# Kernel tuning notes

Hardware: AMD Instinct MI355X
Metric: run time of the kernel (lower is better)

## Reference

```python
import jax, jax.numpy as jnp
import numpy as np

NUM_HEADS = 8
EPS = 1e-12  # torch F.normalize default eps


def setup_inputs() -> dict:
    key = jax.random.key(0)
    k0, k1, k2, k3 = jax.random.split(key, 4)
    b, c, d, h, w = 2, 64, 8, 128, 128
    x = jax.random.normal(k0, (b, c, d, h, w), dtype=jnp.float32)
    # 1x1x1 conv weights stored as [out, in]; depthwise 3x3x3 as [out, 1, kd, kh, kw]
    w_qkv = jax.random.normal(k1, (3 * c, c), dtype=jnp.float32) * 0.05
    w_dw = jax.random.normal(k2, (3 * c, 1, 3, 3, 3), dtype=jnp.float32) * 0.05
    temperature = jnp.ones((NUM_HEADS, 1, 1), dtype=jnp.float32)
    w_proj = jax.random.normal(k3, (c, c), dtype=jnp.float32) * 0.05
    return {"x": x, "w_qkv": w_qkv, "w_dw": w_dw, "temperature": temperature, "w_proj": w_proj}


def _l2norm(t):
    # F.normalize(t, dim=-1): t / max(||t||, eps)
    n = jnp.sqrt(jnp.sum(t * t, axis=-1, keepdims=True))
    return t / jnp.maximum(n, EPS)


def reference(x, w_qkv, w_dw, temperature, w_proj):
    b, c, d, h, w = x.shape
    heads = NUM_HEADS
    ch = c // heads  # per-head channel dim
    # 1x1x1 conv (pointwise) -> einsum over channels
    qkv = jnp.einsum('bcdhw,oc->bodhw', x, w_qkv)
    # depthwise 3x3x3 conv, padding 1 (SAME), groups = 3*c
    qkv = jax.lax.conv_general_dilated(
        qkv, w_dw, window_strides=(1, 1, 1), padding=[(1, 1)] * 3,
        feature_group_count=3 * c,
        dimension_numbers=('NCDHW', 'OIDHW', 'NCDHW'))
    q, k, v = jnp.split(qkv, 3, axis=1)
    n = d * h * w
    q = q.reshape(b, heads, ch, n)
    k = k.reshape(b, heads, ch, n)
    v = v.reshape(b, heads, ch, n)
    q = _l2norm(q)
    k = _l2norm(k)
    # channel-channel attention: [b, heads, ch, ch]
    attn = jnp.einsum('bhcn,bhen->bhce', q, k) * temperature
    attn = jax.nn.softmax(attn, axis=-1)
    out = jnp.einsum('bhce,bhen->bhcn', attn, v)
    out = out.reshape(b, c, d, h, w)
    out = jnp.einsum('bcdhw,oc->bodhw', out, w_proj)
    return out
```

## Files before the change

kernel.cpp:

```cpp
#include <hip/hip_runtime.h>
#include <math.h>

#define NPOS 131072
#define GC 128

typedef __attribute__((ext_vector_type(8))) short short8v;
typedef __attribute__((ext_vector_type(4))) float f32x4;

__device__ __forceinline__ void bf16split(float x, unsigned short& hi, unsigned short& lo) {
  unsigned u = __float_as_uint(x);
  hi = (unsigned short)(u >> 16);
  float hif = __uint_as_float(u & 0xffff0000u);
  float l = x - hif;
  lo = (unsigned short)(__float_as_uint(l) >> 16);
}

__global__ void k_prep(const float* __restrict__ w_qkv, unsigned short* __restrict__ whi,
                       unsigned short* __restrict__ wlo) {
  int idx = blockIdx.x * 256 + threadIdx.x;
  if (idx < 12288) {
    int j = idx & 7, l = (idx >> 3) & 63, ks = (idx >> 9) & 1, ot = (idx >> 10) & 3,
        g = idx >> 12;
    int out = ot * 16 + (l & 15);
    int k = ks * 32 + (l >> 4) * 8 + j;
    bf16split(w_qkv[(g * 64 + out) * 64 + k], whi[idx], wlo[idx]);
  }
}

__device__ __forceinline__ void pw_body(const float* __restrict__ gin,
                                        const short8v (*ahi)[2], const short8v (*alo)[2],
                                        float* __restrict__ gout, int tid) {
  __shared__ __align__(16) float xl[64][66];
  const int lane = tid & 63;
  const int wid = tid >> 6;
  const int f4 = tid & 15;
#pragma unroll
  for (int r = 0; r < 4; ++r) {
    int ch2 = (r * 256 + tid) >> 4;
    *(float4*)&xl[ch2][f4 * 4] = *(const float4*)&gin[(size_t)ch2 * NPOS + f4 * 4];
  }
  __syncthreads();
  const int prow = lane & 15, kgrp = lane >> 4;
  const int pos = wid * 16 + prow;
  short8v bh[2], bl[2];
#pragma unroll
  for (int ks = 0; ks < 2; ++ks)
#pragma unroll
    for (int j = 0; j < 8; ++j) {
      unsigned short h, lo16;
      bf16split(xl[ks * 32 + kgrp * 8 + j][pos], h, lo16);
      bh[ks][j] = (short)h;
      bl[ks][j] = (short)lo16;
    }
  f32x4 D[4];
#pragma unroll
  for (int ot = 0; ot < 4; ++ot) {
    f32x4 d = {0.f, 0.f, 0.f, 0.f};
#pragma unroll
    for (int ks = 0; ks < 2; ++ks) {
      d = __builtin_amdgcn_mfma_f32_16x16x32_bf16(ahi[ot][ks], bh[ks], d, 0, 0, 0);
      d = __builtin_amdgcn_mfma_f32_16x16x32_bf16(ahi[ot][ks], bl[ks], d, 0, 0, 0);
      d = __builtin_amdgcn_mfma_f32_16x16x32_bf16(alo[ot][ks], bh[ks], d, 0, 0, 0);
    }
    D[ot] = d;
  }
  __syncthreads();
#pragma unroll
  for (int ot = 0; ot < 4; ++ot)
#pragma unroll
    for (int jj = 0; jj < 4; ++jj)
      xl[ot * 16 + kgrp * 4 + jj][pos] = D[ot][jj];
  __syncthreads();
#pragma unroll
  for (int r = 0; r < 4; ++r) {
    int row = (r * 256 + tid) >> 4;
    *(float4*)&gout[(size_t)row * NPOS + f4 * 4] = *(const float4*)&xl[row][f4 * 4];
  }
}

__global__ __launch_bounds__(256) void k_pw_mfma(const float* __restrict__ x,
                                                 const unsigned short* __restrict__ whi,
                                                 const unsigned short* __restrict__ wlo,
                                                 float* __restrict__ pre) {
  const int id = blockIdx.x;
  const int sid = (id & 7) * 512 + (id >> 3);
  const int b = sid >> 11;
  const int p0 = (sid & 2047) * 64;
  const int lane = threadIdx.x & 63;
  short8v ahi[4][2], alo[4][2];
#pragma unroll
  for (int ot = 0; ot < 4; ++ot)
#pragma unroll
    for (int ks = 0; ks < 2; ++ks) {
      int fi = ((ot * 2 + ks) * 64 + lane) * 8;
      ahi[ot][ks] = *(const short8v*)&whi[fi];
      alo[ot][ks] = *(const short8v*)&wlo[fi];
    }
  pw_body(x + ((size_t)b * 64) * NPOS + p0, ahi, alo,
          pre + ((size_t)b * 64) * NPOS + p0, threadIdx.x);
}

__device__ __forceinline__ void stage_tile(float (*t)[10][40], const float* __restrict__ in,
                                           int h0, int w0, int tid) {
  for (int i = tid; i < 800; i += 256) {
    int j = i & 7, row = i >> 3;
    int h = row % 10, dpl = row / 10;
    int dd = dpl - 1, hh = h0 + h - 1;
    float4 v = make_float4(0.f, 0.f, 0.f, 0.f);
    if (dd >= 0 && dd < 8 && hh >= 0 && hh < 128)
      v = *(const float4*)&in[((size_t)dd * 128 + hh) * 128 + (w0 + j * 4)];
    *(float4*)&t[dpl][h][4 + j * 4] = v;
  }
  for (int i = tid; i < 200; i += 256) {
    int side = i & 1, row = i >> 1;
    int h = row % 10, dpl = row / 10;
    int dd = dpl - 1, hh = h0 + h - 1;
    int ww = side ? (w0 + 32) : (w0 - 1);
    float v = 0.f;
    if (dd >= 0 && dd < 8 && hh >= 0 && hh < 128 && ww >= 0 && ww < 128)
      v = in[((size_t)dd * 128 + hh) * 128 + ww];
    t[dpl][h][side ? 36 : 3] = v;
  }
}

__device__ __forceinline__ void conv_droll(const float (*t)[10][40], const float* wk,
                                           int hl, int wl, float* acc) {
#pragma unroll
  for (int d = 0; d < 8; ++d) acc[d] = 0.f;
#pragma unroll
  for (int dpl = 0; dpl < 10; ++dpl) {
#pragma unroll
    for (int kh = 0; kh < 3; ++kh) {
#pragma unroll
      for (int kw = 0; kw < 3; ++kw) {
        float f = t[dpl][hl + kh][3 + wl + kw];
#pragma unroll
        for (int kd = 0; kd < 3; ++kd) {
          const int d = dpl - kd;
          if (d >= 0 && d < 8)
            acc[d] = fmaf(f, wk[(kd * 3 + kh) * 3 + kw], acc[d]);
        }
      }
    }
  }
}

__global__ __launch_bounds__(256) void k_dw(const float* __restrict__ pre,
                                            const float* __restrict__ w_dw,
                                            float* __restrict__ conv,
                                            float* __restrict__ nsq, int g) {
  const int id = blockIdx.x;
  const int sid = (id & 7) * 1024 + (id >> 3);
  const int z = sid >> 6, r = sid & 63, by = r >> 2, bx = r & 3;
  const int b = z >> 6;
  const int c = z & 63;
  const int h0 = by * 8;
  const int w0 = bx * 32;
  __shared__ float t[10][10][40];
  __shared__ float red[4];
  const int tid = threadIdx.y * 32 + threadIdx.x;
  stage_tile(t, pre + ((size_t)b * 64 + c) * NPOS, h0, w0, tid);
  float wk[27];
#pragma unroll
  for (int i = 0; i < 27; ++i) wk[i] = w_dw[(g * 64 + c) * 27 + i];
  __syncthreads();
  const int wl = threadIdx.x, hl = threadIdx.y;
  float acc[8];
  conv_droll(t, wk, hl, wl, acc);
  float* outp = conv + ((size_t)b * 64 + c) * NPOS + (size_t)(h0 + hl) * 128 + (w0 + wl);
  float nsum = 0.f;
#pragma unroll
  for (int d = 0; d < 8; ++d) {
    outp[(size_t)d * 16384] = acc[d];
    nsum = fmaf(acc[d], acc[d], nsum);
  }
  if (nsq) {
    const int lane = tid & 63, wv = tid >> 6;
    float v = nsum;
    v += __shfl_down(v, 32); v += __shfl_down(v, 16); v += __shfl_down(v, 8);
    v += __shfl_down(v, 4);  v += __shfl_down(v, 2);  v += __shfl_down(v, 1);
    if (lane == 0) red[wv] = v;
    __syncthreads();
    if (tid == 0) {
      const int blk = by * 4 + bx;
      nsq[((size_t)b * 64 + c) * 64 + blk] = red[0] + red[1] + red[2] + red[3];
    }
  }
}

__global__ __launch_bounds__(256) void k_gramS(const float* __restrict__ qconv,
                                               const float* __restrict__ kconv,
                                               float* __restrict__ partialS) {
  const int chunk = blockIdx.x;
  const int bh = blockIdx.y;
  const int b = bh >> 3, head = bh & 7;
  const int tid = threadIdx.x;
  const size_t base = ((size_t)b * 64 + head * 8) * NPOS + (size_t)chunk * 1024 + tid;
  const float* qb = qconv + base;
  const float* kb = kconv + base;
  float S[64];
#pragma unroll
  for (int i = 0; i < 64; ++i) S[i] = 0.f;
#pragma unroll
  for (int it = 0; it < 4; ++it) {
    const size_t off = (size_t)it * 256;
    float qv[8], kv[8];
#pragma unroll
    for (int c = 0; c < 8; ++c) qv[c] = qb[(size_t)c * NPOS + off];
#pragma unroll
    for (int e = 0; e < 8; ++e) kv[e] = kb[(size_t)e * NPOS + off];
#pragma unroll
    for (int c = 0; c < 8; ++c)
#pragma unroll
      for (int e = 0; e < 8; ++e) S[c * 8 + e] = fmaf(qv[c], kv[e], S[c * 8 + e]);
  }
#pragma unroll
  for (int i = 0; i < 64; ++i) asm volatile("" : "+v"(S[i]));

  const int lane = tid & 63, wv = tid >> 6;
#define BSTEP(src, dst, n, s)                                        \
  {                                                                  \
    const bool hi_ = (lane >> (s)) & 1;                              \
    _Pragma("unroll")                                                \
    for (int i_ = 0; i_ < (n); ++i_) {                               \
      float send_ = hi_ ? src[i_] : src[i_ + (n)];                   \
      float mine_ = hi_ ? src[i_ + (n)] : src[i_];                   \
      dst[i_] = mine_ + __shfl_xor(send_, 1 << (s));                 \
    }                                                                \
  }
  float v32[32], v16[16], v8[8], v4[4], v2[2], v1[1];
  BSTEP(S,   v32, 32, 0)
  BSTEP(v32, v16, 16, 1)
  BSTEP(v16, v8,   8, 2)
  BSTEP(v8,  v4,   4, 3)
  BSTEP(v4,  v2,   2, 4)
  BSTEP(v2,  v1,   1, 5)
#undef BSTEP
  const int idx = ((lane & 1) << 5) | ((lane & 2) << 3) | ((lane & 4) << 1) |
                  ((lane & 8) >> 1) | ((lane & 16) >> 3) | ((lane & 32) >> 5);
  __shared__ float red[4][64];
  red[wv][idx] = v1[0];
  __syncthreads();
  if (tid < 64) {
    float s = red[0][tid] + red[1][tid] + red[2][tid] + red[3][tid];
    partialS[((size_t)bh * GC + chunk) * 64 + tid] = s;
  }
}

__global__ void k_attn(const float* __restrict__ partialS, const float* __restrict__ nqp,
                       const float* __restrict__ nkp, const float* __restrict__ temp,
                       float* __restrict__ A) {
  const int bh = blockIdx.x;
  const int b = bh >> 3, head = bh & 7;
  const int tid = threadIdx.x;
  __shared__ float sums[80];
  if (tid < 64) {
    float s = 0.f;
    const float* pp = partialS + (size_t)bh * GC * 64 + tid;
    for (int j = 0; j < GC; ++j) s += pp[j * 64];
    sums[tid] = s;
  } else if (tid < 72) {
    const int e = tid - 64;
    float s = 0.f;
    const float* pp = nkp + ((size_t)b * 64 + head * 8 + e) * 64;
    for (int j = 0; j < 64; ++j) s += pp[j];
    sums[64 + e] = s;
  } else if (tid < 80) {
    const int c = tid - 72;
    float s = 0.f;
    const float* pp = nqp + ((size_t)b * 64 + head * 8 + c) * 64;
    for (int j = 0; j < 64; ++j) s += pp[j];
    sums[72 + c] = s;
  }
  __syncthreads();
  if (tid < 8) {
    const int c = tid;
    float tp = temp[head];
    float qd = fmaxf(sqrtf(sums[72 + c]), 1e-12f);
    float vals[8];
    float mx = -1e30f;
#pragma unroll
    for (int e = 0; e < 8; ++e) {
      float kd = fmaxf(sqrtf(sums[64 + e]), 1e-12f);
      vals[e] = sums[c * 8 + e] / (qd * kd) * tp;
      mx = fmaxf(mx, vals[e]);
    }
    float den = 0.f;
#pragma unroll
    for (int e = 0; e < 8; ++e) { vals[e] = expf(vals[e] - mx); den += vals[e]; }
#pragma unroll
    for (int e = 0; e < 8; ++e) A[bh * 64 + c * 8 + e] = vals[e] / den;
  }
}

__global__ void k_M(const float* __restrict__ w_proj, const float* __restrict__ A,
                    unsigned short* __restrict__ Mhi, unsigned short* __restrict__ Mlo) {
  const int b = blockIdx.x;
  for (int e = threadIdx.x; e < 4096; e += 256) {
    int j = e & 7, l = (e >> 3) & 63, ks = (e >> 9) & 1, ot = (e >> 10) & 3;
    int out = ot * 16 + (l & 15);
    int gch = ks * 32 + (l >> 4) * 8 + j;
    int hg = gch >> 3, jj = gch & 7;
    float s = 0.f;
#pragma unroll
    for (int i = 0; i < 8; ++i)
      s += w_proj[out * 64 + hg * 8 + i] * A[(b * 8 + hg) * 64 + i * 8 + jj];
    bf16split(s, Mhi[b * 4096 + e], Mlo[b * 4096 + e]);
  }
}

__global__ __launch_bounds__(256) void k_out_mfma(const float* __restrict__ vconv,
                                                  const unsigned short* __restrict__ Mhi,
                                                  const unsigned short* __restrict__ Mlo,
                                                  float* __restrict__ out) {
  const int id = blockIdx.x;
  const int sid = (id & 7) * 512 + (id >> 3);
  const int b = sid >> 11;
  const int p0 = (sid & 2047) * 64;
  const int lane = threadIdx.x & 63;
  short8v ahi[4][2], alo[4][2];
#pragma unroll
  for (int ot = 0; ot < 4; ++ot)
#pragma unroll
    for (int ks = 0; ks < 2; ++ks) {
      int fi = b * 4096 + ((ot * 2 + ks) * 64 + lane) * 8;
      ahi[ot][ks] = *(const short8v*)&Mhi[fi];
      alo[ot][ks] = *(const short8v*)&Mlo[fi];
    }
  pw_body(vconv + ((size_t)b * 64) * NPOS + p0, ahi, alo,
          out + ((size_t)b * 64) * NPOS + p0, threadIdx.x);
}

extern "C" void kernel_launch(void* const* d_in, const int* in_sizes, int n_in,
                              void* d_out, int out_size, void* d_ws, size_t ws_size,
                              hipStream_t stream) {
  const float* x      = (const float*)d_in[0];
  const float* w_qkv  = (const float*)d_in[1];
  const float* w_dw   = (const float*)d_in[2];
  const float* temp   = (const float*)d_in[3];
  const float* w_proj = (const float*)d_in[4];
  float* out = (float*)d_out;
  float* ws  = (float*)d_ws;

  float* conv_buf = ws;
  float* kconv    = conv_buf + 16777216ull;
  float* nqp      = kconv + 16777216ull;
  float* nkp      = nqp + 8192ull;
  float* partialS = nkp + 8192ull;
  float* Abuf     = partialS + 131072ull;
  unsigned short* whi = (unsigned short*)(Abuf + 1024ull);
  unsigned short* wlo = whi + 12288ull;
  unsigned short* Mhi = wlo + 12288ull;
  unsigned short* Mlo = Mhi + 8192ull;

  k_prep<<<48, 256, 0, stream>>>(w_qkv, whi, wlo);
  k_pw_mfma<<<4096, 256, 0, stream>>>(x, whi, wlo, out);
  k_dw<<<8192, dim3(32, 8), 0, stream>>>(out, w_dw, conv_buf, nqp, 0);
  k_pw_mfma<<<4096, 256, 0, stream>>>(x, whi + 4096, wlo + 4096, out);
  k_dw<<<8192, dim3(32, 8), 0, stream>>>(out, w_dw, kconv, nkp, 1);
  k_gramS<<<dim3(GC, 16), 256, 0, stream>>>(conv_buf, kconv, partialS);
  k_attn<<<16, 128, 0, stream>>>(partialS, nqp, nkp, temp, Abuf);
  k_M<<<2, 256, 0, stream>>>(w_proj, Abuf, Mhi, Mlo);
  k_pw_mfma<<<4096, 256, 0, stream>>>(x, whi + 8192, wlo + 8192, out);
  k_dw<<<8192, dim3(32, 8), 0, stream>>>(out, w_dw, conv_buf, nullptr, 2);
  k_out_mfma<<<4096, 256, 0, stream>>>(conv_buf, Mhi, Mlo, out);
}
```

Measured before the change: 224.8 us.

## Store intermediate buffers in position-blocked layout [b][tile][c][64]

```diff
diff --git a/kernel.cpp b/kernel.cpp
--- a/kernel.cpp
+++ b/kernel.cpp
@@ -6,6 +6,10 @@
 
 typedef __attribute__((ext_vector_type(8))) short short8v;
 typedef __attribute__((ext_vector_type(4))) float f32x4;
+
+__device__ __forceinline__ size_t baddr(int b, int c, int p) {
+  return ((size_t)(b * 2048 + (p >> 6)) * 64 + c) * 64 + (p & 63);
+}
 
 __device__ __forceinline__ void bf16split(float x, unsigned short& hi, unsigned short& lo) {
   unsigned u = __float_as_uint(x);
@@ -27,19 +31,10 @@
   }
 }
 
-__device__ __forceinline__ void pw_body(const float* __restrict__ gin,
-                                        const short8v (*ahi)[2], const short8v (*alo)[2],
-                                        float* __restrict__ gout, int tid) {
-  __shared__ __align__(16) float xl[64][66];
+__device__ __forceinline__ void pw_mfma_core(float (*xl)[66], const short8v (*ahi)[2],
+                                             const short8v (*alo)[2], int tid) {
   const int lane = tid & 63;
   const int wid = tid >> 6;
-  const int f4 = tid & 15;
-#pragma unroll
-  for (int r = 0; r < 4; ++r) {
-    int ch2 = (r * 256 + tid) >> 4;
-    *(float4*)&xl[ch2][f4 * 4] = *(const float4*)&gin[(size_t)ch2 * NPOS + f4 * 4];
-  }
-  __syncthreads();
   const int prow = lane & 15, kgrp = lane >> 4;
   const int pos = wid * 16 + prow;
   short8v bh[2], bl[2];
@@ -71,11 +66,6 @@
     for (int jj = 0; jj < 4; ++jj)
       xl[ot * 16 + kgrp * 4 + jj][pos] = D[ot][jj];
   __syncthreads();
-#pragma unroll
-  for (int r = 0; r < 4; ++r) {
-    int row = (r * 256 + tid) >> 4;
-    *(float4*)&gout[(size_t)row * NPOS + f4 * 4] = *(const float4*)&xl[row][f4 * 4];
-  }
 }
 
 __global__ __launch_bounds__(256) void k_pw_mfma(const float* __restrict__ x,
@@ -85,8 +75,12 @@
   const int id = blockIdx.x;
   const int sid = (id & 7) * 512 + (id >> 3);
   const int b = sid >> 11;
-  const int p0 = (sid & 2047) * 64;
+  const int t = sid & 2047;
+  const int p0 = t * 64;
   const int lane = threadIdx.x & 63;
+  const int tid = threadIdx.x;
+  const int f4 = tid & 15;
+  __shared__ __align__(16) float xl[64][66];
   short8v ahi[4][2], alo[4][2];
 #pragma unroll
   for (int ot = 0; ot < 4; ++ot)
@@ -96,52 +90,19 @@
       ahi[ot][ks] = *(const short8v*)&whi[fi];
       alo[ot][ks] = *(const short8v*)&wlo[fi];
     }
-  pw_body(x + ((size_t)b * 64) * NPOS + p0, ahi, alo,
-          pre + ((size_t)b * 64) * NPOS + p0, threadIdx.x);
-}
-
-__device__ __forceinline__ void stage_tile(float (*t)[10][40], const float* __restrict__ in,
-                                           int h0, int w0, int tid) {
-  for (int i = tid; i < 800; i += 256) {
-    int j = i & 7, row = i >> 3;
-    int h = row % 10, dpl = row / 10;
-    int dd = dpl - 1, hh = h0 + h - 1;
-    float4 v = make_float4(0.f, 0.f, 0.f, 0.f);
-    if (dd >= 0 && dd < 8 && hh >= 0 && hh < 128)
-      v = *(const float4*)&in[((size_t)dd * 128 + hh) * 128 + (w0 + j * 4)];
-    *(float4*)&t[dpl][h][4 + j * 4] = v;
-  }
-  for (int i = tid; i < 200; i += 256) {
-    int side = i & 1, row = i >> 1;
-    int h = row % 10, dpl = row / 10;
-    int dd = dpl - 1, hh = h0 + h - 1;
-    int ww = side ? (w0 + 32) : (w0 - 1);
-    float v = 0.f;
-    if (dd >= 0 && dd < 8 && hh >= 0 && hh < 128 && ww >= 0 && ww < 128)
-      v = in[((size_t)dd * 128 + hh) * 128 + ww];
-    t[dpl][h][side ? 36 : 3] = v;
-  }
-}
-
-__device__ __forceinline__ void conv_droll(const float (*t)[10][40], const float* wk,
-                                           int hl, int wl, float* acc) {
-#pragma unroll
-  for (int d = 0; d < 8; ++d) acc[d] = 0.f;
-#pragma unroll
-  for (int dpl = 0; dpl < 10; ++dpl) {
-#pragma unroll
-    for (int kh = 0; kh < 3; ++kh) {
-#pragma unroll
-      for (int kw = 0; kw < 3; ++kw) {
-        float f = t[dpl][hl + kh][3 + wl + kw];
-#pragma unroll
-        for (int kd = 0; kd < 3; ++kd) {
-          const int d = dpl - kd;
-          if (d >= 0 && d < 8)
-            acc[d] = fmaf(f, wk[(kd * 3 + kh) * 3 + kw], acc[d]);
-        }
-      }
-    }
+  const float* xb = x + ((size_t)b * 64) * NPOS + p0;
+#pragma unroll
+  for (int r = 0; r < 4; ++r) {
+    int ch2 = (r * 256 + tid) >> 4;
+    *(float4*)&xl[ch2][f4 * 4] = *(const float4*)&xb[(size_t)ch2 * NPOS + f4 * 4];
+  }
+  __syncthreads();
+  pw_mfma_core(xl, ahi, alo, tid);
+  float* go = pre + ((size_t)(b * 2048 + t) * 64) * 64;
+#pragma unroll
+  for (int r = 0; r < 4; ++r) {
+    int idx = r * 256 + tid;
+    *(float4*)&go[(size_t)idx * 4] = *(const float4*)&xl[idx >> 4][(idx & 15) * 4];
   }
 }
 
@@ -159,19 +120,54 @@
   __shared__ float t[10][10][40];
   __shared__ float red[4];
   const int tid = threadIdx.y * 32 + threadIdx.x;
-  stage_tile(t, pre + ((size_t)b * 64 + c) * NPOS, h0, w0, tid);
+  for (int i = tid; i < 800; i += 256) {
+    int j = i & 7, row = i >> 3;
+    int h = row % 10, dpl = row / 10;
+    int dd = dpl - 1, hh = h0 + h - 1;
+    float4 v = make_float4(0.f, 0.f, 0.f, 0.f);
+    if (dd >= 0 && dd < 8 && hh >= 0 && hh < 128) {
+      int p = dd * 16384 + hh * 128 + w0 + j * 4;
+      v = *(const float4*)&pre[baddr(b, c, p)];
+    }
+    *(float4*)&t[dpl][h][4 + j * 4] = v;
+  }
+  for (int i = tid; i < 200; i += 256) {
+    int side = i & 1, row = i >> 1;
+    int h = row % 10, dpl = row / 10;
+    int dd = dpl - 1, hh = h0 + h - 1;
+    int ww = side ? (w0 + 32) : (w0 - 1);
+    float v = 0.f;
+    if (dd >= 0 && dd < 8 && hh >= 0 && hh < 128 && ww >= 0 && ww < 128)
+      v = pre[baddr(b, c, dd * 16384 + hh * 128 + ww)];
+    t[dpl][h][side ? 36 : 3] = v;
+  }
   float wk[27];
 #pragma unroll
   for (int i = 0; i < 27; ++i) wk[i] = w_dw[(g * 64 + c) * 27 + i];
   __syncthreads();
   const int wl = threadIdx.x, hl = threadIdx.y;
   float acc[8];
-  conv_droll(t, wk, hl, wl, acc);
-  float* outp = conv + ((size_t)b * 64 + c) * NPOS + (size_t)(h0 + hl) * 128 + (w0 + wl);
+#pragma unroll
+  for (int d = 0; d < 8; ++d) acc[d] = 0.f;
+#pragma unroll
+  for (int dpl = 0; dpl < 10; ++dpl)
+#pragma unroll
+    for (int kh = 0; kh < 3; ++kh)
+#pragma unroll
+      for (int kw = 0; kw < 3; ++kw) {
+        float f = t[dpl][hl + kh][3 + wl + kw];
+#pragma unroll
+        for (int kd = 0; kd < 3; ++kd) {
+          const int d = dpl - kd;
+          if (d >= 0 && d < 8)
+            acc[d] = fmaf(f, wk[(kd * 3 + kh) * 3 + kw], acc[d]);
+        }
+      }
   float nsum = 0.f;
 #pragma unroll
   for (int d = 0; d < 8; ++d) {
-    outp[(size_t)d * 16384] = acc[d];
+    int p = d * 16384 + (h0 + hl) * 128 + (w0 + wl);
+    conv[baddr(b, c, p)] = acc[d];
     nsum = fmaf(acc[d], acc[d], nsum);
   }
   if (nsq) {
@@ -195,20 +191,19 @@
   const int bh = blockIdx.y;
   const int b = bh >> 3, head = bh & 7;
   const int tid = threadIdx.x;
-  const size_t base = ((size_t)b * 64 + head * 8) * NPOS + (size_t)chunk * 1024 + tid;
-  const float* qb = qconv + base;
-  const float* kb = kconv + base;
+  const int c0 = head * 8;
   float S[64];
 #pragma unroll
   for (int i = 0; i < 64; ++i) S[i] = 0.f;
 #pragma unroll
   for (int it = 0; it < 4; ++it) {
-    const size_t off = (size_t)it * 256;
+    int p = chunk * 1024 + it * 256 + tid;
+    size_t tbase = ((size_t)(b * 2048 + (p >> 6)) * 64) * 64 + (p & 63);
     float qv[8], kv[8];
 #pragma unroll
-    for (int c = 0; c < 8; ++c) qv[c] = qb[(size_t)c * NPOS + off];
-#pragma unroll
-    for (int e = 0; e < 8; ++e) kv[e] = kb[(size_t)e * NPOS + off];
+    for (int c = 0; c < 8; ++c) qv[c] = qconv[tbase + (size_t)(c0 + c) * 64];
+#pragma unroll
+    for (int e = 0; e < 8; ++e) kv[e] = kconv[tbase + (size_t)(c0 + e) * 64];
 #pragma unroll
     for (int c = 0; c < 8; ++c)
 #pragma unroll
@@ -316,8 +311,12 @@
   const int id = blockIdx.x;
   const int sid = (id & 7) * 512 + (id >> 3);
   const int b = sid >> 11;
-  const int p0 = (sid & 2047) * 64;
+  const int t = sid & 2047;
+  const int p0 = t * 64;
   const int lane = threadIdx.x & 63;
+  const int tid = threadIdx.x;
+  const int f4 = tid & 15;
+  __shared__ __align__(16) float xl[64][66];
   short8v ahi[4][2], alo[4][2];
 #pragma unroll
   for (int ot = 0; ot < 4; ++ot)
@@ -327,8 +326,20 @@
       ahi[ot][ks] = *(const short8v*)&Mhi[fi];
       alo[ot][ks] = *(const short8v*)&Mlo[fi];
     }
-  pw_body(vconv + ((size_t)b * 64) * NPOS + p0, ahi, alo,
-          out + ((size_t)b * 64) * NPOS + p0, threadIdx.x);
+  const float* gi = vconv + ((size_t)(b * 2048 + t) * 64) * 64;
+#pragma unroll
+  for (int r = 0; r < 4; ++r) {
+    int idx = r * 256 + tid;
+    *(float4*)&xl[idx >> 4][(idx & 15) * 4] = *(const float4*)&gi[(size_t)idx * 4];
+  }
+  __syncthreads();
+  pw_mfma_core(xl, ahi, alo, tid);
+  float* ob = out + ((size_t)b * 64) * NPOS + p0;
+#pragma unroll
+  for (int r = 0; r < 4; ++r) {
+    int row = (r * 256 + tid) >> 4;
+    *(float4*)&ob[(size_t)row * NPOS + f4 * 4] = *(const float4*)&xl[row][f4 * 4];
+  }
 }
 
 extern "C" void kernel_launch(void* const* d_in, const int* in_sizes, int n_in,
```

After: 234.5 us. 1.04x slower.
